# Kernel optimization log

Measured on AMD Instinct MI355X. Metric: run time of the kernel, lower is better.

The kernel has to match this reference:

```python
import jax, jax.numpy as jnp
import numpy as np
import math

B, S, D, H = 8, 1024, 1024, 16
DH = D // H  # 64


def setup_inputs() -> dict:
    key = jax.random.key(0)
    ks = jax.random.split(key, 10)
    inputs = jax.random.normal(ks[0], (B, S, D), dtype=jnp.float32)
    mask = jax.random.randint(ks[1], (B, S, S), 0, 2) == 1  # bool [B,S,S]
    sc = 1.0 / math.sqrt(D)
    # per-head projection weights stacked: [H, D, DH], biases [H, DH]
    Wq = jax.random.normal(ks[2], (H, D, DH), dtype=jnp.float32) * sc
    bq = jax.random.normal(ks[3], (H, DH), dtype=jnp.float32) * 0.02
    Wk = jax.random.normal(ks[4], (H, D, DH), dtype=jnp.float32) * sc
    bk = jax.random.normal(ks[5], (H, DH), dtype=jnp.float32) * 0.02
    Wv = jax.random.normal(ks[6], (H, D, DH), dtype=jnp.float32) * sc
    bv = jax.random.normal(ks[7], (H, DH), dtype=jnp.float32) * 0.02
    Wo = jax.random.normal(ks[8], (D, D), dtype=jnp.float32) * sc
    bo = jax.random.normal(ks[9], (D,), dtype=jnp.float32) * 0.02
    return {"inputs": inputs, "mask": mask, "Wq": Wq, "bq": bq, "Wk": Wk,
            "bk": bk, "Wv": Wv, "bv": bv, "Wo": Wo, "bo": bo}


def reference(inputs, mask, Wq, bq, Wk, bk, Wv, bv, Wo, bo):
    d_model = inputs.shape[-1]
    scale = 1.0 / jnp.sqrt(jnp.asarray(d_model, inputs.dtype))  # note: sqrt(d_model), as in source
    # batched per-head projections: [B,H,S,DH]
    Q = jnp.einsum('bsd,hde->bhse', inputs, Wq) + bq[None, :, None, :]
    K = jnp.einsum('bsd,hde->bhse', inputs, Wk) + bk[None, :, None, :]
    V = jnp.einsum('bsd,hde->bhse', inputs, Wv) + bv[None, :, None, :]
    scores = jnp.einsum('bhse,bhte->bhst', Q, K) * scale  # [B,H,S,S]
    scores = jnp.where(mask[:, None, :, :], jnp.asarray(-1e9, scores.dtype), scores)
    attn = jax.nn.softmax(scores, axis=-1)
    ctx = jnp.einsum('bhst,bhte->bhse', attn, V)  # [B,H,S,DH]
    # concat heads along last dim (head h -> slice h*DH:(h+1)*DH), matches torch.cat
    bsz, h, s, dh = ctx.shape
    x = ctx.transpose(0, 2, 1, 3).reshape(bsz, s, h * dh)
    return x @ Wo + bo
```

## Files before the change

kernel.cpp:

```cpp
#include <hip/hip_runtime.h>
#include <hip/hip_bf16.h>
#include <stdint.h>


typedef __attribute__((ext_vector_type(8))) short short8;
typedef __attribute__((ext_vector_type(4))) float floatx4;

#define C2S 0.04508422f

__device__ __forceinline__ int swz(int r, int kc) { return r * 8 + (kc ^ (r & 7)); }
__device__ __forceinline__ short8 as_frag(uint4 u) { return __builtin_bit_cast(short8, u); }
__device__ __forceinline__ floatx4 mfma16(short8 a, short8 b, floatx4 c) {
    return __builtin_amdgcn_mfma_f32_16x16x32_bf16(a, b, c, 0, 0, 0);
}
__device__ __forceinline__ unsigned short f2bu(float f) {
    return __builtin_bit_cast(unsigned short, __float2bfloat16(f));
}
__device__ __forceinline__ short f2b(float f) {
    return __builtin_bit_cast(short, __float2bfloat16(f));
}
__device__ __forceinline__ float b2f(short s) {
    return __bfloat162float(__builtin_bit_cast(__hip_bfloat16, s));
}
__device__ __forceinline__ void dma16(const void* g, void* l) {
    __builtin_amdgcn_global_load_lds(
        (const __attribute__((address_space(1))) uint32_t*)g,
        (__attribute__((address_space(3))) uint32_t*)l, 16, 0, 0);
}
__device__ __forceinline__ uint2 pack4(float a, float b, float c, float d) {
    uint2 p;
    p.x = (unsigned)f2bu(a) | ((unsigned)f2bu(b) << 16);
    p.y = (unsigned)f2bu(c) | ((unsigned)f2bu(d) << 16);
    return p;
}

__device__ __forceinline__ void detect_mode(const unsigned* Xw, int* s_is32) {
    if (threadIdx.x < 64) {
        unsigned lo = Xw[threadIdx.x] & 0xFFFFu;
        unsigned e = (lo >> 7) & 0xFFu;
        unsigned long long bal = __ballot(e >= 88u && e <= 150u);
        if (threadIdx.x == 0) *s_is32 = (bal != ~0ull) ? 1 : 0;
    }
    __syncthreads();
}

__device__ __forceinline__ float load_elt(const void* p, size_t idx, int is32) {
    return is32 ? ((const float*)p)[idx]
                : __bfloat162float(((const __hip_bfloat16*)p)[idx]);
}

__global__ __launch_bounds__(256) void prep_all(
    const void* __restrict__ Wq, const void* __restrict__ Wk,
    const void* __restrict__ Wv, const void* __restrict__ Wo,
    const void* __restrict__ bq, const void* __restrict__ bk,
    const void* __restrict__ bv, const void* __restrict__ bo,
    const void* __restrict__ mask_raw, const void* __restrict__ X,
    __hip_bfloat16* __restrict__ WT, __hip_bfloat16* __restrict__ WoT,
    __hip_bfloat16* __restrict__ bc, unsigned long long* __restrict__ bits64,
    __hip_bfloat16* __restrict__ Xb, int do_x)
{
    __shared__ __hip_bfloat16 T[64][72];
    __shared__ int s_is32;
    int blk = blockIdx.x;
    int tid = threadIdx.x;
    const unsigned* Xw = (const unsigned*)X;

    if (blk < 1024) {
        detect_mode(Xw, &s_is32);
        const void* src; size_t src_off;
        __hip_bfloat16* dst;
        int src_ld, dst_ld;
        if (blk < 768) {
            int p = blk >> 8;
            int rem = blk & 255;
            int h = rem >> 4, dt = rem & 15;
            src = (p == 0) ? Wq : (p == 1) ? Wk : Wv;
            src_off = ((size_t)h * 1024 + (size_t)dt * 64) * 64;
            dst = WT + (((size_t)p * 16 + h) * 64) * 1024 + dt * 64;
            src_ld = 64; dst_ld = 1024;
        } else {
            int t = blk - 768;
            int kt = t >> 4, nt = t & 15;
            src = Wo; src_off = (size_t)kt * 64 * 1024 + nt * 64;
            dst = WoT + (size_t)nt * 64 * 1024 + kt * 64;
            src_ld = 1024; dst_ld = 1024;
        }
        #pragma unroll
        for (int i = 0; i < 16; i++) {
            int idx = tid + i * 256;
            int r = idx >> 6, c = idx & 63;
            T[c][r] = __float2bfloat16(load_elt(src, src_off + (size_t)r * src_ld + c, s_is32));
        }
        __syncthreads();
        #pragma unroll
        for (int i = 0; i < 16; i++) {
            int idx = tid + i * 256;
            int r = idx >> 6, c = idx & 63;
            dst[(size_t)r * dst_ld + c] = T[r][c];
        }
    } else if (blk == 1024) {
        detect_mode(Xw, &s_is32);
        #pragma unroll
        for (int i = 0; i < 16; i++) {
            int idx = tid + i * 256;
            int which = idx >> 10, j = idx & 1023;
            const void* src = (which == 0) ? bq : (which == 1) ? bk : (which == 2) ? bv : bo;
            float v = load_elt(src, j, s_is32);
            if (which == 0) v *= C2S;
            bc[idx] = __float2bfloat16(v);
        }
    } else if (blk < 1537) {
        int blkL = blk - 1025;
        const int* mi = (const int*)mask_raw;
        const unsigned char* mb = (const unsigned char*)mask_raw;
        int lane = tid & 63;
        bool ok = true;
        #pragma unroll
        for (int i = 0; i < 4; i++) {
            unsigned v = (unsigned)mi[lane * 4 + i];
            if (v > 1u) ok = false;
        }
        bool is_i32 = (__ballot(ok) == ~0ull);
        int gw = (blkL * 256 + tid) >> 6;
        const int NW = 512 * 4;
        const int NWORDS = (8 * 1024 * 1024) / 64;
        if (is_i32) {
            for (int i = gw; i < NWORDS; i += NW) {
                int mv = mi[(size_t)i * 64 + lane];
                unsigned long long bal = __ballot(mv != 0);
                if (lane == 0) {
                    int bb = i >> 14, q = (i >> 4) & 1023, t = i & 15;
                    bits64[((size_t)bb << 14) + ((size_t)t << 10) + q] = bal;
                }
            }
        } else {
            for (int i = gw; i < NWORDS; i += NW) {
                int mv = mb[(size_t)i * 64 + lane];
                unsigned long long bal = __ballot(mv != 0);
                if (lane == 0) {
                    int bb = i >> 14, q = (i >> 4) & 1023, t = i & 15;
                    bits64[((size_t)bb << 14) + ((size_t)t << 10) + q] = bal;
                }
            }
        }
    } else if (do_x) {
        detect_mode(Xw, &s_is32);
        int blkL = blk - 1537;
        size_t g = ((size_t)blkL * 256 + tid) * 16;
        if (s_is32) {
            const float* Xf = (const float*)X;
            #pragma unroll
            for (int half = 0; half < 2; half++) {
                float4 f0 = *(const float4*)(Xf + g + half * 8);
                float4 f1 = *(const float4*)(Xf + g + half * 8 + 4);
                short8 s;
                s[0] = f2b(f0.x); s[1] = f2b(f0.y); s[2] = f2b(f0.z); s[3] = f2b(f0.w);
                s[4] = f2b(f1.x); s[5] = f2b(f1.y); s[6] = f2b(f1.z); s[7] = f2b(f1.w);
                *(uint4*)(Xb + g + half * 8) = __builtin_bit_cast(uint4, s);
            }
        } else {
            const uint4* Xu = (const uint4*)X;
            *(uint4*)(Xb + g)     = Xu[g / 8];
            *(uint4*)(Xb + g + 8) = Xu[g / 8 + 1];
        }
    }
}

__global__ __launch_bounds__(256, 2) void qkv_gemm_dma(
    const __hip_bfloat16* __restrict__ Xb,
    const __hip_bfloat16* __restrict__ WT,
    const __hip_bfloat16* __restrict__ bc,
    __hip_bfloat16* __restrict__ Q,
    __hip_bfloat16* __restrict__ Ko,
    __hip_bfloat16* __restrict__ Vt)
{
    __shared__ uint4 AsU[256 * 8];
    __shared__ uint4 BsU[128 * 8];
    int tid = threadIdx.x, lane = tid & 63, wave = tid >> 6;
    int quad = lane >> 4, ln = lane & 15;
    int mw = wave & 1, nw = wave >> 1;
    int m0 = blockIdx.x * 256;
    int n0 = blockIdx.y * 128;
    const __hip_bfloat16* Wp = WT + (size_t)n0 * 1024;

    floatx4 acc[8][4];
    #pragma unroll
    for (int i = 0; i < 8; i++)
        #pragma unroll
        for (int j = 0; j < 4; j++) acc[i][j] = (floatx4){0.f, 0.f, 0.f, 0.f};

    for (int k0 = 0; k0 < 1024; k0 += 64) {
        #pragma unroll
        for (int i = 0; i < 8; i++) {
            int r = wave * 64 + i * 8 + (lane >> 3);
            int kc = (lane & 7) ^ (r & 7);
            char* lds = (char*)AsU + (size_t)(wave * 512 + i * 64) * 16;
            dma16(Xb + (size_t)(m0 + r) * 1024 + k0 + kc * 8, lds);
        }
        #pragma unroll
        for (int i = 0; i < 4; i++) {
            int r = wave * 32 + i * 8 + (lane >> 3);
            int kc = (lane & 7) ^ (r & 7);
            char* lds = (char*)BsU + (size_t)(wave * 256 + i * 64) * 16;
            dma16(Wp + (size_t)r * 1024 + k0 + kc * 8, lds);
        }
        __syncthreads();
        #pragma unroll
        for (int kk = 0; kk < 2; kk++) {
            short8 af[8], bf[4];
            #pragma unroll
            for (int mi = 0; mi < 8; mi++)
                af[mi] = as_frag(AsU[swz(mw * 128 + mi * 16 + ln, kk * 4 + quad)]);
            #pragma unroll
            for (int ni = 0; ni < 4; ni++)
                bf[ni] = as_frag(BsU[swz(nw * 64 + ni * 16 + ln, kk * 4 + quad)]);
            #pragma unroll
            for (int mi = 0; mi < 8; mi++)
                #pragma unroll
                for (int ni = 0; ni < 4; ni++)
                    acc[mi][ni] = mfma16(af[mi], bf[ni], acc[mi][ni]);
        }
        __syncthreads();
    }

    int b = m0 >> 10;
    int s0 = m0 & 1023;
    int proj = n0 >> 10;
    if (proj == 2) {
        #pragma unroll
        for (int ni = 0; ni < 4; ni++) {
            int n = n0 + nw * 64 + ni * 16 + ln;
            int h = (n >> 6) & 15, e = n & 63;
            float bval = __bfloat162float(bc[2 * 1024 + (n & 1023)]);
            #pragma unroll
            for (int mi = 0; mi < 8; mi++) {
                int sb = s0 + mw * 128 + mi * 16 + quad * 4;
                uint2 pk = pack4(acc[mi][ni][0] + bval, acc[mi][ni][1] + bval,
                                 acc[mi][ni][2] + bval, acc[mi][ni][3] + bval);
                *(uint2*)(Vt + (((size_t)b * 16 + h) * 64 + e) * 1024 + sb) = pk;
            }
        }
    } else {
        __hip_bfloat16* P = (proj == 0) ? Q : Ko;
        float sc = (proj == 0) ? C2S : 1.f;
        #pragma unroll
        for (int ni = 0; ni < 4; ni++) {
            int n = n0 + nw * 64 + ni * 16 + ln;
            int h = (n >> 6) & 15, e = n & 63;
            float bval = __bfloat162float(bc[proj * 1024 + (n & 1023)]);
            #pragma unroll
            for (int mi = 0; mi < 8; mi++) {
                #pragma unroll
                for (int r = 0; r < 4; r++) {
                    int s = s0 + mw * 128 + mi * 16 + quad * 4 + r;
                    P[(((size_t)b * 16 + h) * 1024 + s) * 64 + e] =
                        __float2bfloat16(acc[mi][ni][r] * sc + bval);
                }
            }
        }
    }
}

__global__ __launch_bounds__(256) void qkv_gemm2(
    const void* __restrict__ Xsrc,
    const __hip_bfloat16* __restrict__ WT,
    const __hip_bfloat16* __restrict__ bc,
    __hip_bfloat16* __restrict__ Q,
    __hip_bfloat16* __restrict__ Ko,
    __hip_bfloat16* __restrict__ Vt)
{
    __shared__ int s_is32;
    detect_mode((const unsigned*)Xsrc, &s_is32);
    __shared__ uint4 AsU[128 * 8];
    __shared__ uint4 BsU[128 * 8];
    int tid = threadIdx.x, lane = tid & 63, wave = tid >> 6;
    int quad = lane >> 4, ln = lane & 15;
    int m0 = blockIdx.x * 128;
    int n0 = blockIdx.y * 128;
    const __hip_bfloat16* Wp = WT + (size_t)n0 * 1024;
    const float* Xf = (const float*)Xsrc;
    const __hip_bfloat16* Xh = (const __hip_bfloat16*)Xsrc;

    floatx4 acc[2][8];
    #pragma unroll
    for (int i = 0; i < 2; i++)
        #pragma unroll
        for (int j = 0; j < 8; j++) acc[i][j] = (floatx4){0.f, 0.f, 0.f, 0.f};

    for (int k0 = 0; k0 < 1024; k0 += 64) {
        if (s_is32) {
            #pragma unroll
            for (int i = 0; i < 4; i++) {
                int id = tid + i * 256;
                int r = id >> 3, kc = id & 7;
                size_t off = (size_t)(m0 + r) * 1024 + k0 + kc * 8;
                float4 f0 = *(const float4*)(Xf + off);
                float4 f1 = *(const float4*)(Xf + off + 4);
                short8 s;
                s[0] = f2b(f0.x); s[1] = f2b(f0.y); s[2] = f2b(f0.z); s[3] = f2b(f0.w);
                s[4] = f2b(f1.x); s[5] = f2b(f1.y); s[6] = f2b(f1.z); s[7] = f2b(f1.w);
                AsU[swz(r, kc)] = __builtin_bit_cast(uint4, s);
            }
        } else {
            #pragma unroll
            for (int i = 0; i < 4; i++) {
                int id = tid + i * 256;
                int r = id >> 3, kc = id & 7;
                AsU[swz(r, kc)] = *(const uint4*)(Xh + (size_t)(m0 + r) * 1024 + k0 + kc * 8);
            }
        }
        #pragma unroll
        for (int i = 0; i < 4; i++) {
            int id = tid + i * 256;
            int r = id >> 3, kc = id & 7;
            BsU[swz(r, kc)] = *(const uint4*)(Wp + (size_t)r * 1024 + k0 + kc * 8);
        }
        __syncthreads();
        #pragma unroll
        for (int kk = 0; kk < 2; kk++) {
            short8 a0 = as_frag(AsU[swz(wave * 32 + ln, kk * 4 + quad)]);
            short8 a1 = as_frag(AsU[swz(wave * 32 + 16 + ln, kk * 4 + quad)]);
            #pragma unroll
            for (int nt = 0; nt < 8; nt++) {
                short8 bf = as_frag(BsU[swz(nt * 16 + ln, kk * 4 + quad)]);
                acc[0][nt] = mfma16(a0, bf, acc[0][nt]);
                acc[1][nt] = mfma16(a1, bf, acc[1][nt]);
            }
        }
        __syncthreads();
    }

    int b = m0 >> 10;
    int s0 = m0 & 1023;
    #pragma unroll
    for (int nt = 0; nt < 8; nt++) {
        int n = n0 + nt * 16 + ln;
        int proj = n >> 10, h = (n >> 6) & 15, e = n & 63;
        float bval = __bfloat162float(bc[proj * 1024 + (n & 1023)]);
        float sc = (proj == 0) ? C2S : 1.f;
        #pragma unroll
        for (int mt = 0; mt < 2; mt++) {
            #pragma unroll
            for (int r = 0; r < 4; r++) {
                int s = s0 + wave * 32 + mt * 16 + quad * 4 + r;
                float v = acc[mt][nt][r] * sc + bval;
                if (proj == 2) {
                    Vt[(((size_t)b * 16 + h) * 64 + e) * 1024 + s] = __float2bfloat16(v);
                } else {
                    __hip_bfloat16* P = (proj == 0) ? Q : Ko;
                    P[(((size_t)b * 16 + h) * 1024 + s) * 64 + e] = __float2bfloat16(v);
                }
            }
        }
    }
}

__global__ __launch_bounds__(512, 4) void attn(
    const __hip_bfloat16* __restrict__ Q,
    const __hip_bfloat16* __restrict__ K,
    const __hip_bfloat16* __restrict__ Vt,
    const unsigned long long* __restrict__ bits,
    __hip_bfloat16* __restrict__ ctx)
{
    __shared__ uint4 KsU[2 * 512];
    __shared__ uint4 VsU[2 * 512];
    __shared__ uint4 PsU[8 * 256];

    int tid = threadIdx.x, lane = tid & 63, w = tid >> 6;
    int quad = lane >> 4, ln = lane & 15;
    int bh = blockIdx.x;
    int q0 = blockIdx.y * 256;
    int b = bh >> 4, h = bh & 15;
    const __hip_bfloat16* Qp = Q + (size_t)bh * 1024 * 64;
    const __hip_bfloat16* Kp = K + (size_t)bh * 1024 * 64;
    const __hip_bfloat16* Vp = Vt + (size_t)bh * 64 * 1024;
    const unsigned long long* bp = bits + (size_t)b * 16 * 1024;

    short8 qf[2][2];
    #pragma unroll
    for (int g = 0; g < 2; g++)
        #pragma unroll
        for (int kk = 0; kk < 2; kk++)
            qf[g][kk] = as_frag(*(const uint4*)(
                Qp + (size_t)(q0 + w * 32 + g * 16 + ln) * 64 + kk * 32 + quad * 8));

    int r8 = lane >> 3;
    int kc = (lane & 7) ^ r8;

    floatx4 acc_o[2][4];
    #pragma unroll
    for (int g = 0; g < 2; g++)
        #pragma unroll
        for (int i = 0; i < 4; i++) acc_o[g][i] = (floatx4){0.f, 0.f, 0.f, 0.f};
    float lsum[2] = {0.f, 0.f};
    __hip_bfloat16* Pw = (__hip_bfloat16*)&PsU[w * 256];

    for (int t0 = 0; t0 < 1024; t0 += 128) {
        __syncthreads();
        #pragma unroll
        for (int i = 0; i < 2; i++) {
            int tK = t0 + i * 64 + w * 8 + r8;
            dma16(Kp + (size_t)tK * 64 + kc * 8,
                  (char*)KsU + (size_t)(i * 512 + w * 64) * 16);
            int e = w * 8 + r8;
            dma16(Vp + (size_t)e * 1024 + t0 + i * 64 + kc * 8,
                  (char*)VsU + (size_t)(i * 512 + w * 64) * 16);
        }
        __syncthreads();

        #pragma unroll
        for (int s = 0; s < 2; s++) {
            int t64 = (t0 >> 6) + s;
            unsigned long long mcur0 = bp[((size_t)t64 << 10) + q0 + w * 32 + ln];
            unsigned long long mcur1 = bp[((size_t)t64 << 10) + q0 + w * 32 + 16 + ln];
            const uint4* Ks = KsU + s * 512;
            const uint4* Vs = VsU + s * 512;

            floatx4 st[2][4];
            #pragma unroll
            for (int g = 0; g < 2; g++)
                #pragma unroll
                for (int i = 0; i < 4; i++) st[g][i] = (floatx4){0.f, 0.f, 0.f, 0.f};
            __builtin_amdgcn_s_setprio(1);
            #pragma unroll
            for (int kk = 0; kk < 2; kk++) {
                #pragma unroll
                for (int tt = 0; tt < 4; tt++) {
                    short8 kf = as_frag(Ks[swz(tt * 16 + ln, kk * 4 + quad)]);
                    st[0][tt] = mfma16(kf, qf[0][kk], st[0][tt]);
                    st[1][tt] = mfma16(kf, qf[1][kk], st[1][tt]);
                }
            }
            __builtin_amdgcn_s_setprio(0);

            #pragma unroll
            for (int g = 0; g < 2; g++) {
                int qloc = g * 16 + ln;
                unsigned long long msh = (g ? mcur1 : mcur0) >> (quad * 4);
                #pragma unroll
                for (int tt = 0; tt < 4; tt++) {
                    unsigned mb = (unsigned)(msh >> (tt * 16)) & 0xFu;
                    float pe0 = (mb & 1u) ? 0.f : __builtin_amdgcn_exp2f(st[g][tt][0]);
                    float pe1 = (mb & 2u) ? 0.f : __builtin_amdgcn_exp2f(st[g][tt][1]);
                    float pe2 = (mb & 4u) ? 0.f : __builtin_amdgcn_exp2f(st[g][tt][2]);
                    float pe3 = (mb & 8u) ? 0.f : __builtin_amdgcn_exp2f(st[g][tt][3]);
                    lsum[g] += (pe0 + pe1) + (pe2 + pe3);
                    int kcp = tt * 2 + (quad >> 1);
                    int off = qloc * 64 + (kcp ^ (qloc & 7)) * 8 + (quad & 1) * 4;
                    *(uint2*)(Pw + off) = pack4(pe0, pe1, pe2, pe3);
                }
            }

            __builtin_amdgcn_s_setprio(1);
            #pragma unroll
            for (int kk = 0; kk < 2; kk++) {
                short8 pf0 = as_frag(PsU[w * 256 + swz(0 * 16 + ln, kk * 4 + quad)]);
                short8 pf1 = as_frag(PsU[w * 256 + swz(1 * 16 + ln, kk * 4 + quad)]);
                #pragma unroll
                for (int et = 0; et < 4; et++) {
                    short8 vf = as_frag(Vs[swz(et * 16 + ln, kk * 4 + quad)]);
                    acc_o[0][et] = mfma16(vf, pf0, acc_o[0][et]);
                    acc_o[1][et] = mfma16(vf, pf1, acc_o[1][et]);
                }
            }
            __builtin_amdgcn_s_setprio(0);
        }
    }

    #pragma unroll
    for (int g = 0; g < 2; g++) {
        lsum[g] += __shfl_xor(lsum[g], 16, 64);
        lsum[g] += __shfl_xor(lsum[g], 32, 64);
    }

    #pragma unroll
    for (int g = 0; g < 2; g++) {
        float inv = 1.f / fmaxf(lsum[g], 1e-20f);
        int s = q0 + w * 32 + g * 16 + ln;
        __hip_bfloat16* crow = ctx + ((size_t)b * 1024 + s) * 1024 + h * 64 + quad * 4;
        #pragma unroll
        for (int et = 0; et < 4; et++) {
            uint2 pk = pack4(acc_o[g][et][0] * inv, acc_o[g][et][1] * inv,
                             acc_o[g][et][2] * inv, acc_o[g][et][3] * inv);
            *(uint2*)(crow + et * 16) = pk;
        }
    }
}

__global__ __launch_bounds__(256) void out_gemm_dma(
    const __hip_bfloat16* __restrict__ Cx,
    const __hip_bfloat16* __restrict__ WoT,
    const __hip_bfloat16* __restrict__ bc,
    const unsigned* __restrict__ Xw,
    void* __restrict__ dout,
    int direct)
{
    __shared__ int s_is32;
    detect_mode(Xw, &s_is32);
    __shared__ uint4 AsU[128 * 8];
    __shared__ uint4 BsU[128 * 8];
    int tid = threadIdx.x, lane = tid & 63, wave = tid >> 6;
    int quad = lane >> 4, ln = lane & 15;
    int mw = wave & 1, nw = wave >> 1;
    int m0 = blockIdx.x * 128;
    int n0 = blockIdx.y * 128;

    floatx4 acc[4][4];
    #pragma unroll
    for (int i = 0; i < 4; i++)
        #pragma unroll
        for (int j = 0; j < 4; j++) acc[i][j] = (floatx4){0.f, 0.f, 0.f, 0.f};

    for (int k0 = 0; k0 < 1024; k0 += 64) {
        #pragma unroll
        for (int i = 0; i < 4; i++) {
            int r = wave * 32 + i * 8 + (lane >> 3);
            int kc = (lane & 7) ^ (r & 7);
            char* ldsA = (char*)AsU + (size_t)(wave * 256 + i * 64) * 16;
            char* ldsB = (char*)BsU + (size_t)(wave * 256 + i * 64) * 16;
            dma16(Cx + (size_t)(m0 + r) * 1024 + k0 + kc * 8, ldsA);
            dma16(WoT + (size_t)(n0 + r) * 1024 + k0 + kc * 8, ldsB);
        }
        __syncthreads();
        #pragma unroll
        for (int kk = 0; kk < 2; kk++) {
            short8 af[4], bf[4];
            #pragma unroll
            for (int mi = 0; mi < 4; mi++)
                af[mi] = as_frag(AsU[swz(mw * 64 + mi * 16 + ln, kk * 4 + quad)]);
            #pragma unroll
            for (int ni = 0; ni < 4; ni++)
                bf[ni] = as_frag(BsU[swz(nw * 64 + ni * 16 + ln, kk * 4 + quad)]);
            #pragma unroll
            for (int mi = 0; mi < 4; mi++)
                #pragma unroll
                for (int ni = 0; ni < 4; ni++)
                    acc[mi][ni] = mfma16(af[mi], bf[ni], acc[mi][ni]);
        }
        __syncthreads();
    }

    const __hip_bfloat16* bo = bc + 3 * 1024;
    #pragma unroll
    for (int ni = 0; ni < 4; ni++) {
        int n = n0 + nw * 64 + ni * 16 + ln;
        float bval = __bfloat162float(bo[n]);
        #pragma unroll
        for (int mi = 0; mi < 4; mi++) {
            #pragma unroll
            for (int r = 0; r < 4; r++) {
                int m = m0 + mw * 64 + mi * 16 + quad * 4 + r;
                float v = acc[mi][ni][r] + bval;
                if (direct && s_is32) ((float*)dout)[(size_t)m * 1024 + n] = v;
                else ((__hip_bfloat16*)dout)[(size_t)m * 1024 + n] = __float2bfloat16(v);
            }
        }
    }
}

__global__ __launch_bounds__(256) void emit_out(
    const __hip_bfloat16* __restrict__ Fo, const unsigned* __restrict__ Xw,
    void* __restrict__ dout)
{
    __shared__ int s_is32;
    detect_mode(Xw, &s_is32);
    size_t g = (size_t)blockIdx.x * 256 + threadIdx.x;
    uint4 u = *(const uint4*)(Fo + g * 8);
    if (s_is32) {
        short8 s = __builtin_bit_cast(short8, u);
        float4 f0, f1;
        f0.x = b2f(s[0]); f0.y = b2f(s[1]); f0.z = b2f(s[2]); f0.w = b2f(s[3]);
        f1.x = b2f(s[4]); f1.y = b2f(s[5]); f1.z = b2f(s[6]); f1.w = b2f(s[7]);
        *(float4*)((float*)dout + g * 8) = f0;
        *(float4*)((float*)dout + g * 8 + 4) = f1;
    } else {
        *(uint4*)((__hip_bfloat16*)dout + g * 8) = u;
    }
}

extern "C" void kernel_launch(void* const* d_in, const int* in_sizes, int n_in,
                              void* d_out, int out_size, void* d_ws, size_t ws_size,
                              hipStream_t stream) {
    const void* X  = d_in[0];
    const void* mk = d_in[1];
    const void* Wq = d_in[2];
    const void* bq = d_in[3];
    const void* Wk = d_in[4];
    const void* bk = d_in[5];
    const void* Wv = d_in[6];
    const void* bv = d_in[7];
    const void* Wo = d_in[8];
    const void* bo = d_in[9];
    const unsigned* Xw = (const unsigned*)X;

    char* ws = (char*)d_ws;
    __hip_bfloat16*     WT   = (__hip_bfloat16*)(ws);
    __hip_bfloat16*     WoT  = (__hip_bfloat16*)(ws + ((size_t)6 << 20));
    unsigned long long* bits = (unsigned long long*)(ws + ((size_t)8 << 20));
    __hip_bfloat16*     bc   = (__hip_bfloat16*)(ws + ((size_t)9 << 20));
    __hip_bfloat16*     Xb   = (__hip_bfloat16*)(ws + ((size_t)10 << 20));
    __hip_bfloat16*     Qb   = (__hip_bfloat16*)(ws + ((size_t)26 << 20));
    __hip_bfloat16*     Kb   = (__hip_bfloat16*)(ws + ((size_t)42 << 20));
    __hip_bfloat16*     Vtb  = (__hip_bfloat16*)(ws + ((size_t)58 << 20));

    bool bigws = ws_size >= ((size_t)74 << 20);

    hipLaunchKernelGGL(prep_all, dim3(3585), dim3(256), 0, stream,
                       Wq, Wk, Wv, Wo, bq, bk, bv, bo, mk, X,
                       WT, WoT, bc, bits, Xb, bigws ? 1 : 0);

    if (bigws) {
        __hip_bfloat16* Cx = Xb;
        hipLaunchKernelGGL(qkv_gemm_dma, dim3(32, 24), dim3(256), 0, stream,
                           Xb, WT, bc, Qb, Kb, Vtb);
        hipLaunchKernelGGL(attn, dim3(128, 4), dim3(512), 0, stream,
                           Qb, Kb, Vtb, bits, Cx);
        hipLaunchKernelGGL(out_gemm_dma, dim3(64, 8), dim3(256), 0, stream,
                           Cx, WoT, bc, Xw, d_out, 1);
    } else {
        __hip_bfloat16* Cx = (__hip_bfloat16*)d_out;
        __hip_bfloat16* Fo = Qb;
        hipLaunchKernelGGL(qkv_gemm2, dim3(64, 24), dim3(256), 0, stream,
                           X, WT, bc, Qb, Kb, Vtb);
        hipLaunchKernelGGL(attn, dim3(128, 4), dim3(512), 0, stream,
                           Qb, Kb, Vtb, bits, Cx);
        hipLaunchKernelGGL(out_gemm_dma, dim3(64, 8), dim3(256), 0, stream,
                           Cx, WoT, bc, Xw, (void*)Fo, 0);
        hipLaunchKernelGGL(emit_out, dim3(4096), dim3(256), 0, stream,
                           Fo, Xw, d_out);
    }
}
```

Baseline: 307.3 us.

## Fuse fp32-to-bf16 conversion of X into QKV GEMM and enlarge output GEMM tile

Removes the separate pass in prep_all that converted X to a bf16 workspace copy. The QKV GEMM now reads fp32 X directly, converts it in registers and writes it into the swizzled LDS tile, while W tiles still arrive by global-to-LDS DMA. This saves a full write and re-read of X in global memory, but the fp32 path now uses per-thread loads instead of DMA. The output GEMM also moves from 128x128 to 256x128 tiles, which gives more reuse per block but halves the grid to 256 blocks.

```diff
diff --git a/kernel.cpp b/kernel.cpp
--- a/kernel.cpp
+++ b/kernel.cpp
@@ -32,6 +32,12 @@
     p.x = (unsigned)f2bu(a) | ((unsigned)f2bu(b) << 16);
     p.y = (unsigned)f2bu(c) | ((unsigned)f2bu(d) << 16);
     return p;
+}
+__device__ __forceinline__ short8 cvt8(float4 f0, float4 f1) {
+    short8 s;
+    s[0] = f2b(f0.x); s[1] = f2b(f0.y); s[2] = f2b(f0.z); s[3] = f2b(f0.w);
+    s[4] = f2b(f1.x); s[5] = f2b(f1.y); s[6] = f2b(f1.z); s[7] = f2b(f1.w);
+    return s;
 }
 
 __device__ __forceinline__ void detect_mode(const unsigned* Xw, int* s_is32) {
@@ -56,8 +62,7 @@
     const void* __restrict__ bv, const void* __restrict__ bo,
     const void* __restrict__ mask_raw, const void* __restrict__ X,
     __hip_bfloat16* __restrict__ WT, __hip_bfloat16* __restrict__ WoT,
-    __hip_bfloat16* __restrict__ bc, unsigned long long* __restrict__ bits64,
-    __hip_bfloat16* __restrict__ Xb, int do_x)
+    __hip_bfloat16* __restrict__ bc, unsigned long long* __restrict__ bits64)
 {
     __shared__ __hip_bfloat16 T[64][72];
     __shared__ int s_is32;
@@ -109,7 +114,7 @@
             if (which == 0) v *= C2S;
             bc[idx] = __float2bfloat16(v);
         }
-    } else if (blk < 1537) {
+    } else {
         int blkL = blk - 1025;
         const int* mi = (const int*)mask_raw;
         const unsigned char* mb = (const unsigned char*)mask_raw;
@@ -143,125 +148,10 @@
                 }
             }
         }
-    } else if (do_x) {
-        detect_mode(Xw, &s_is32);
-        int blkL = blk - 1537;
-        size_t g = ((size_t)blkL * 256 + tid) * 16;
-        if (s_is32) {
-            const float* Xf = (const float*)X;
-            #pragma unroll
-            for (int half = 0; half < 2; half++) {
-                float4 f0 = *(const float4*)(Xf + g + half * 8);
-                float4 f1 = *(const float4*)(Xf + g + half * 8 + 4);
-                short8 s;
-                s[0] = f2b(f0.x); s[1] = f2b(f0.y); s[2] = f2b(f0.z); s[3] = f2b(f0.w);
-                s[4] = f2b(f1.x); s[5] = f2b(f1.y); s[6] = f2b(f1.z); s[7] = f2b(f1.w);
-                *(uint4*)(Xb + g + half * 8) = __builtin_bit_cast(uint4, s);
-            }
-        } else {
-            const uint4* Xu = (const uint4*)X;
-            *(uint4*)(Xb + g)     = Xu[g / 8];
-            *(uint4*)(Xb + g + 8) = Xu[g / 8 + 1];
-        }
-    }
-}
-
-__global__ __launch_bounds__(256, 2) void qkv_gemm_dma(
-    const __hip_bfloat16* __restrict__ Xb,
-    const __hip_bfloat16* __restrict__ WT,
-    const __hip_bfloat16* __restrict__ bc,
-    __hip_bfloat16* __restrict__ Q,
-    __hip_bfloat16* __restrict__ Ko,
-    __hip_bfloat16* __restrict__ Vt)
-{
-    __shared__ uint4 AsU[256 * 8];
-    __shared__ uint4 BsU[128 * 8];
-    int tid = threadIdx.x, lane = tid & 63, wave = tid >> 6;
-    int quad = lane >> 4, ln = lane & 15;
-    int mw = wave & 1, nw = wave >> 1;
-    int m0 = blockIdx.x * 256;
-    int n0 = blockIdx.y * 128;
-    const __hip_bfloat16* Wp = WT + (size_t)n0 * 1024;
-
-    floatx4 acc[8][4];
-    #pragma unroll
-    for (int i = 0; i < 8; i++)
-        #pragma unroll
-        for (int j = 0; j < 4; j++) acc[i][j] = (floatx4){0.f, 0.f, 0.f, 0.f};
-
-    for (int k0 = 0; k0 < 1024; k0 += 64) {
-        #pragma unroll
-        for (int i = 0; i < 8; i++) {
-            int r = wave * 64 + i * 8 + (lane >> 3);
-            int kc = (lane & 7) ^ (r & 7);
-            char* lds = (char*)AsU + (size_t)(wave * 512 + i * 64) * 16;
-            dma16(Xb + (size_t)(m0 + r) * 1024 + k0 + kc * 8, lds);
-        }
-        #pragma unroll
-        for (int i = 0; i < 4; i++) {
-            int r = wave * 32 + i * 8 + (lane >> 3);
-            int kc = (lane & 7) ^ (r & 7);
-            char* lds = (char*)BsU + (size_t)(wave * 256 + i * 64) * 16;
-            dma16(Wp + (size_t)r * 1024 + k0 + kc * 8, lds);
-        }
-        __syncthreads();
-        #pragma unroll
-        for (int kk = 0; kk < 2; kk++) {
-            short8 af[8], bf[4];
-            #pragma unroll
-            for (int mi = 0; mi < 8; mi++)
-                af[mi] = as_frag(AsU[swz(mw * 128 + mi * 16 + ln, kk * 4 + quad)]);
-            #pragma unroll
-            for (int ni = 0; ni < 4; ni++)
-                bf[ni] = as_frag(BsU[swz(nw * 64 + ni * 16 + ln, kk * 4 + quad)]);
-            #pragma unroll
-            for (int mi = 0; mi < 8; mi++)
-                #pragma unroll
-                for (int ni = 0; ni < 4; ni++)
-                    acc[mi][ni] = mfma16(af[mi], bf[ni], acc[mi][ni]);
-        }
-        __syncthreads();
-    }
-
-    int b = m0 >> 10;
-    int s0 = m0 & 1023;
-    int proj = n0 >> 10;
-    if (proj == 2) {
-        #pragma unroll
-        for (int ni = 0; ni < 4; ni++) {
-            int n = n0 + nw * 64 + ni * 16 + ln;
-            int h = (n >> 6) & 15, e = n & 63;
-            float bval = __bfloat162float(bc[2 * 1024 + (n & 1023)]);
-            #pragma unroll
-            for (int mi = 0; mi < 8; mi++) {
-                int sb = s0 + mw * 128 + mi * 16 + quad * 4;
-                uint2 pk = pack4(acc[mi][ni][0] + bval, acc[mi][ni][1] + bval,
-                                 acc[mi][ni][2] + bval, acc[mi][ni][3] + bval);
-                *(uint2*)(Vt + (((size_t)b * 16 + h) * 64 + e) * 1024 + sb) = pk;
-            }
-        }
-    } else {
-        __hip_bfloat16* P = (proj == 0) ? Q : Ko;
-        float sc = (proj == 0) ? C2S : 1.f;
-        #pragma unroll
-        for (int ni = 0; ni < 4; ni++) {
-            int n = n0 + nw * 64 + ni * 16 + ln;
-            int h = (n >> 6) & 15, e = n & 63;
-            float bval = __bfloat162float(bc[proj * 1024 + (n & 1023)]);
-            #pragma unroll
-            for (int mi = 0; mi < 8; mi++) {
-                #pragma unroll
-                for (int r = 0; r < 4; r++) {
-                    int s = s0 + mw * 128 + mi * 16 + quad * 4 + r;
-                    P[(((size_t)b * 16 + h) * 1024 + s) * 64 + e] =
-                        __float2bfloat16(acc[mi][ni][r] * sc + bval);
-                }
-            }
-        }
-    }
-}
-
-__global__ __launch_bounds__(256) void qkv_gemm2(
+    }
+}
+
+__global__ __launch_bounds__(256, 2) void qkv_gemm(
     const void* __restrict__ Xsrc,
     const __hip_bfloat16* __restrict__ WT,
     const __hip_bfloat16* __restrict__ bc,
@@ -271,84 +161,102 @@
 {
     __shared__ int s_is32;
     detect_mode((const unsigned*)Xsrc, &s_is32);
-    __shared__ uint4 AsU[128 * 8];
+    __shared__ uint4 AsU[256 * 8];
     __shared__ uint4 BsU[128 * 8];
     int tid = threadIdx.x, lane = tid & 63, wave = tid >> 6;
     int quad = lane >> 4, ln = lane & 15;
-    int m0 = blockIdx.x * 128;
+    int mw = wave & 1, nw = wave >> 1;
+    int m0 = blockIdx.x * 256;
     int n0 = blockIdx.y * 128;
     const __hip_bfloat16* Wp = WT + (size_t)n0 * 1024;
     const float* Xf = (const float*)Xsrc;
     const __hip_bfloat16* Xh = (const __hip_bfloat16*)Xsrc;
-
-    floatx4 acc[2][8];
-    #pragma unroll
-    for (int i = 0; i < 2; i++)
-        #pragma unroll
-        for (int j = 0; j < 8; j++) acc[i][j] = (floatx4){0.f, 0.f, 0.f, 0.f};
+    int is32 = s_is32;
+
+    floatx4 acc[8][4];
+    #pragma unroll
+    for (int i = 0; i < 8; i++)
+        #pragma unroll
+        for (int j = 0; j < 4; j++) acc[i][j] = (floatx4){0.f, 0.f, 0.f, 0.f};
 
     for (int k0 = 0; k0 < 1024; k0 += 64) {
-        if (s_is32) {
-            #pragma unroll
-            for (int i = 0; i < 4; i++) {
-                int id = tid + i * 256;
-                int r = id >> 3, kc = id & 7;
+        #pragma unroll
+        for (int i = 0; i < 4; i++) {
+            int r = wave * 32 + i * 8 + (lane >> 3);
+            int kc = (lane & 7) ^ (r & 7);
+            char* lds = (char*)BsU + (size_t)(wave * 256 + i * 64) * 16;
+            dma16(Wp + (size_t)r * 1024 + k0 + kc * 8, lds);
+        }
+        if (is32) {
+            #pragma unroll
+            for (int i = 0; i < 8; i++) {
+                int r = wave * 64 + i * 8 + (lane >> 3);
+                int kc = (lane & 7) ^ (r & 7);
                 size_t off = (size_t)(m0 + r) * 1024 + k0 + kc * 8;
                 float4 f0 = *(const float4*)(Xf + off);
                 float4 f1 = *(const float4*)(Xf + off + 4);
-                short8 s;
-                s[0] = f2b(f0.x); s[1] = f2b(f0.y); s[2] = f2b(f0.z); s[3] = f2b(f0.w);
-                s[4] = f2b(f1.x); s[5] = f2b(f1.y); s[6] = f2b(f1.z); s[7] = f2b(f1.w);
-                AsU[swz(r, kc)] = __builtin_bit_cast(uint4, s);
+                AsU[wave * 512 + i * 64 + lane] = __builtin_bit_cast(uint4, cvt8(f0, f1));
             }
         } else {
             #pragma unroll
-            for (int i = 0; i < 4; i++) {
-                int id = tid + i * 256;
-                int r = id >> 3, kc = id & 7;
-                AsU[swz(r, kc)] = *(const uint4*)(Xh + (size_t)(m0 + r) * 1024 + k0 + kc * 8);
-            }
-        }
-        #pragma unroll
-        for (int i = 0; i < 4; i++) {
-            int id = tid + i * 256;
-            int r = id >> 3, kc = id & 7;
-            BsU[swz(r, kc)] = *(const uint4*)(Wp + (size_t)r * 1024 + k0 + kc * 8);
+            for (int i = 0; i < 8; i++) {
+                int r = wave * 64 + i * 8 + (lane >> 3);
+                int kc = (lane & 7) ^ (r & 7);
+                char* lds = (char*)AsU + (size_t)(wave * 512 + i * 64) * 16;
+                dma16(Xh + (size_t)(m0 + r) * 1024 + k0 + kc * 8, lds);
+            }
         }
         __syncthreads();
         #pragma unroll
         for (int kk = 0; kk < 2; kk++) {
-            short8 a0 = as_frag(AsU[swz(wave * 32 + ln, kk * 4 + quad)]);
-            short8 a1 = as_frag(AsU[swz(wave * 32 + 16 + ln, kk * 4 + quad)]);
-            #pragma unroll
-            for (int nt = 0; nt < 8; nt++) {
-                short8 bf = as_frag(BsU[swz(nt * 16 + ln, kk * 4 + quad)]);
-                acc[0][nt] = mfma16(a0, bf, acc[0][nt]);
-                acc[1][nt] = mfma16(a1, bf, acc[1][nt]);
-            }
+            short8 af[8], bf[4];
+            #pragma unroll
+            for (int mi = 0; mi < 8; mi++)
+                af[mi] = as_frag(AsU[swz(mw * 128 + mi * 16 + ln, kk * 4 + quad)]);
+            #pragma unroll
+            for (int ni = 0; ni < 4; ni++)
+                bf[ni] = as_frag(BsU[swz(nw * 64 + ni * 16 + ln, kk * 4 + quad)]);
+            #pragma unroll
+            for (int mi = 0; mi < 8; mi++)
+                #pragma unroll
+                for (int ni = 0; ni < 4; ni++)
+                    acc[mi][ni] = mfma16(af[mi], bf[ni], acc[mi][ni]);
         }
         __syncthreads();
     }
 
     int b = m0 >> 10;
     int s0 = m0 & 1023;
-    #pragma unroll
-    for (int nt = 0; nt < 8; nt++) {
-        int n = n0 + nt * 16 + ln;
-        int proj = n >> 10, h = (n >> 6) & 15, e = n & 63;
-        float bval = __bfloat162float(bc[proj * 1024 + (n & 1023)]);
+    int proj = n0 >> 10;
+    if (proj == 2) {
+        #pragma unroll
+        for (int ni = 0; ni < 4; ni++) {
+            int n = n0 + nw * 64 + ni * 16 + ln;
+            int h = (n >> 6) & 15, e = n & 63;
+            float bval = __bfloat162float(bc[2 * 1024 + (n & 1023)]);
+            #pragma unroll
+            for (int mi = 0; mi < 8; mi++) {
+                int sb = s0 + mw * 128 + mi * 16 + quad * 4;
+                uint2 pk = pack4(acc[mi][ni][0] + bval, acc[mi][ni][1] + bval,
+                                 acc[mi][ni][2] + bval, acc[mi][ni][3] + bval);
+                *(uint2*)(Vt + (((size_t)b * 16 + h) * 64 + e) * 1024 + sb) = pk;
+            }
+        }
+    } else {
+        __hip_bfloat16* P = (proj == 0) ? Q : Ko;
         float sc = (proj == 0) ? C2S : 1.f;
         #pragma unroll
-        for (int mt = 0; mt < 2; mt++) {
-            #pragma unroll
-            for (int r = 0; r < 4; r++) {
-                int s = s0 + wave * 32 + mt * 16 + quad * 4 + r;
-                float v = acc[mt][nt][r] * sc + bval;
-                if (proj == 2) {
-                    Vt[(((size_t)b * 16 + h) * 64 + e) * 1024 + s] = __float2bfloat16(v);
-                } else {
-                    __hip_bfloat16* P = (proj == 0) ? Q : Ko;
-                    P[(((size_t)b * 16 + h) * 1024 + s) * 64 + e] = __float2bfloat16(v);
+        for (int ni = 0; ni < 4; ni++) {
+            int n = n0 + nw * 64 + ni * 16 + ln;
+            int h = (n >> 6) & 15, e = n & 63;
+            float bval = __bfloat162float(bc[proj * 1024 + (n & 1023)]);
+            #pragma unroll
+            for (int mi = 0; mi < 8; mi++) {
+                #pragma unroll
+                for (int r = 0; r < 4; r++) {
+                    int s = s0 + mw * 128 + mi * 16 + quad * 4 + r;
+                    P[(((size_t)b * 16 + h) * 1024 + s) * 64 + e] =
+                        __float2bfloat16(acc[mi][ni][r] * sc + bval);
                 }
             }
         }
@@ -487,7 +395,7 @@
     }
 }
 
-__global__ __launch_bounds__(256) void out_gemm_dma(
+__global__ __launch_bounds__(256, 2) void out_gemm_dma(
     const __hip_bfloat16* __restrict__ Cx,
     const __hip_bfloat16* __restrict__ WoT,
     const __hip_bfloat16* __restrict__ bc,
@@ -497,42 +405,48 @@
 {
     __shared__ int s_is32;
     detect_mode(Xw, &s_is32);
-    __shared__ uint4 AsU[128 * 8];
+    __shared__ uint4 AsU[256 * 8];
     __shared__ uint4 BsU[128 * 8];
     int tid = threadIdx.x, lane = tid & 63, wave = tid >> 6;
     int quad = lane >> 4, ln = lane & 15;
     int mw = wave & 1, nw = wave >> 1;
-    int m0 = blockIdx.x * 128;
+    int m0 = blockIdx.x * 256;
     int n0 = blockIdx.y * 128;
-
-    floatx4 acc[4][4];
-    #pragma unroll
-    for (int i = 0; i < 4; i++)
+    const __hip_bfloat16* Wp = WoT + (size_t)n0 * 1024;
+
+    floatx4 acc[8][4];
+    #pragma unroll
+    for (int i = 0; i < 8; i++)
         #pragma unroll
         for (int j = 0; j < 4; j++) acc[i][j] = (floatx4){0.f, 0.f, 0.f, 0.f};
 
     for (int k0 = 0; k0 < 1024; k0 += 64) {
+        #pragma unroll
+        for (int i = 0; i < 8; i++) {
+            int r = wave * 64 + i * 8 + (lane >> 3);
+            int kc = (lane & 7) ^ (r & 7);
+            char* lds = (char*)AsU + (size_t)(wave * 512 + i * 64) * 16;
+            dma16(Cx + (size_t)(m0 + r) * 1024 + k0 + kc * 8, lds);
+        }
         #pragma unroll
         for (int i = 0; i < 4; i++) {
             int r = wave * 32 + i * 8 + (lane >> 3);
             int kc = (lane & 7) ^ (r & 7);
-            char* ldsA = (char*)AsU + (size_t)(wave * 256 + i * 64) * 16;
-            char* ldsB = (char*)BsU + (size_t)(wave * 256 + i * 64) * 16;
-            dma16(Cx + (size_t)(m0 + r) * 1024 + k0 + kc * 8, ldsA);
-            dma16(WoT + (size_t)(n0 + r) * 1024 + k0 + kc * 8, ldsB);
+            char* lds = (char*)BsU + (size_t)(wave * 256 + i * 64) * 16;
+            dma16(Wp + (size_t)r * 1024 + k0 + kc * 8, lds);
         }
         __syncthreads();
         #pragma unroll
         for (int kk = 0; kk < 2; kk++) {
-            short8 af[4], bf[4];
-            #pragma unroll
-            for (int mi = 0; mi < 4; mi++)
-                af[mi] = as_frag(AsU[swz(mw * 64 + mi * 16 + ln, kk * 4 + quad)]);
+            short8 af[8], bf[4];
+            #pragma unroll
+            for (int mi = 0; mi < 8; mi++)
+                af[mi] = as_frag(AsU[swz(mw * 128 + mi * 16 + ln, kk * 4 + quad)]);
             #pragma unroll
             for (int ni = 0; ni < 4; ni++)
                 bf[ni] = as_frag(BsU[swz(nw * 64 + ni * 16 + ln, kk * 4 + quad)]);
             #pragma unroll
-            for (int mi = 0; mi < 4; mi++)
+            for (int mi = 0; mi < 8; mi++)
                 #pragma unroll
                 for (int ni = 0; ni < 4; ni++)
                     acc[mi][ni] = mfma16(af[mi], bf[ni], acc[mi][ni]);
@@ -546,10 +460,10 @@
         int n = n0 + nw * 64 + ni * 16 + ln;
         float bval = __bfloat162float(bo[n]);
         #pragma unroll
-        for (int mi = 0; mi < 4; mi++) {
+        for (int mi = 0; mi < 8; mi++) {
             #pragma unroll
             for (int r = 0; r < 4; r++) {
-                int m = m0 + mw * 64 + mi * 16 + quad * 4 + r;
+                int m = m0 + mw * 128 + mi * 16 + quad * 4 + r;
                 float v = acc[mi][ni][r] + bval;
                 if (direct && s_is32) ((float*)dout)[(size_t)m * 1024 + n] = v;
                 else ((__hip_bfloat16*)dout)[(size_t)m * 1024 + n] = __float2bfloat16(v);
@@ -598,33 +512,31 @@
     __hip_bfloat16*     WoT  = (__hip_bfloat16*)(ws + ((size_t)6 << 20));
     unsigned long long* bits = (unsigned long long*)(ws + ((size_t)8 << 20));
     __hip_bfloat16*     bc   = (__hip_bfloat16*)(ws + ((size_t)9 << 20));
-    __hip_bfloat16*     Xb   = (__hip_bfloat16*)(ws + ((size_t)10 << 20));
+    __hip_bfloat16*     Cxw  = (__hip_bfloat16*)(ws + ((size_t)10 << 20));
     __hip_bfloat16*     Qb   = (__hip_bfloat16*)(ws + ((size_t)26 << 20));
     __hip_bfloat16*     Kb   = (__hip_bfloat16*)(ws + ((size_t)42 << 20));
     __hip_bfloat16*     Vtb  = (__hip_bfloat16*)(ws + ((size_t)58 << 20));
 
     bool bigws = ws_size >= ((size_t)74 << 20);
 
-    hipLaunchKernelGGL(prep_all, dim3(3585), dim3(256), 0, stream,
+    hipLaunchKernelGGL(prep_all, dim3(1537), dim3(256), 0, stream,
                        Wq, Wk, Wv, Wo, bq, bk, bv, bo, mk, X,
-                       WT, WoT, bc, bits, Xb, bigws ? 1 : 0);
+                       WT, WoT, bc, bits);
+
+    hipLaunchKernelGGL(qkv_gemm, dim3(32, 24), dim3(256), 0, stream,
+                       X, WT, bc, Qb, Kb, Vtb);
 
     if (bigws) {
-        __hip_bfloat16* Cx = Xb;
-        hipLaunchKernelGGL(qkv_gemm_dma, dim3(32, 24), dim3(256), 0, stream,
-                           Xb, WT, bc, Qb, Kb, Vtb);
         hipLaunchKernelGGL(attn, dim3(128, 4), dim3(512), 0, stream,
-                           Qb, Kb, Vtb, bits, Cx);
-        hipLaunchKernelGGL(out_gemm_dma, dim3(64, 8), dim3(256), 0, stream,
-                           Cx, WoT, bc, Xw, d_out, 1);
+                           Qb, Kb, Vtb, bits, Cxw);
+        hipLaunchKernelGGL(out_gemm_dma, dim3(32, 8), dim3(256), 0, stream,
+                           Cxw, WoT, bc, Xw, d_out, 1);
     } else {
         __hip_bfloat16* Cx = (__hip_bfloat16*)d_out;
         __hip_bfloat16* Fo = Qb;
-        hipLaunchKernelGGL(qkv_gemm2, dim3(64, 24), dim3(256), 0, stream,
-                           X, WT, bc, Qb, Kb, Vtb);
         hipLaunchKernelGGL(attn, dim3(128, 4), dim3(512), 0, stream,
                            Qb, Kb, Vtb, bits, Cx);
-        hipLaunchKernelGGL(out_gemm_dma, dim3(64, 8), dim3(256), 0, stream,
+        hipLaunchKernelGGL(out_gemm_dma, dim3(32, 8), dim3(256), 0, stream,
                            Cx, WoT, bc, Xw, (void*)Fo, 0);
         hipLaunchKernelGGL(emit_out, dim3(4096), dim3(256), 0, stream,
                            Fo, Xw, d_out);
```

Measured after the change: 331.7 us. 1.08x slower.
